# Optimization experiments

Measured on AMD Instinct MI355X. Metric: run time of the kernel, lower is better.

Reference implementation:

```python
import jax, jax.numpy as jnp
import numpy as np

B, N, K = 8192, 2048, 4  # batch, nodes, neighbors (original: 45, 168, 4)


def _collect_and_transfer(x, adj):
    # x: (B, N), adj: (N, K) int indices of neighbors.
    # Original builds, per node i, a (B, K) block of gathered neighbor values,
    # stacks to (N, B, K), then raw-reshapes (view) to (B, 1, K, N).
    g = jnp.transpose(x[:, adj], (1, 0, 2))   # (N, B, K)
    return g.reshape(x.shape[0], 1, K, adj.shape[0])  # memory reinterpretation, as in .view


def reference(x, label, adj, conv_w, conv_b, lin_w, lin_b):
    a = jnp.concatenate([_collect_and_transfer(x, adj),
                         _collect_and_transfer(label, adj)], axis=1)  # (B, 2, K, N)
    # Conv2d(2 -> 1, kernel=(1,4), stride=(1,4)): (B, 1, K, N//4)
    y = jax.lax.conv_general_dilated(
        a, conv_w, window_strides=(1, 4), padding='VALID',
        dimension_numbers=('NCHW', 'OIHW', 'NCHW'))
    y = jax.nn.relu(y + conv_b[None, :, None, None])
    y = y.reshape(B, N)              # K * (N//4) == N
    return y @ lin_w.T + lin_b       # Linear(N, N)


def setup_inputs() -> dict:
    key = jax.random.key(0)
    k1, k2, k3, k4, k5 = jax.random.split(key, 5)
    return {
        'x': jax.random.normal(k1, (B, N), dtype=jnp.float32),
        'label': jax.random.normal(k2, (B, N), dtype=jnp.float32),
        'adj': jax.random.randint(k3, (N, K), 0, N, dtype=jnp.int32),
        'conv_w': jax.random.normal(k4, (1, 2, 1, 4), dtype=jnp.float32) * 0.1,
        'conv_b': jnp.zeros((1,), dtype=jnp.float32),
        'lin_w': jax.random.normal(k5, (N, N), dtype=jnp.float32) * 0.02,
        'lin_b': jnp.zeros((N,), dtype=jnp.float32),
    }
```

## Files before the change

### kernel.cpp

```cpp
#include <hip/hip_runtime.h>

typedef __bf16 bf16;
typedef bf16 bf16x8 __attribute__((ext_vector_type(8)));
typedef float f32x4 __attribute__((ext_vector_type(4)));
typedef unsigned short ushort;
typedef ushort ushort4v __attribute__((ext_vector_type(4)));

#define BB 8192
#define NN 2048

__device__ __forceinline__ void async16(const void* g, void* l) {
    __builtin_amdgcn_global_load_lds(
        (__attribute__((address_space(1))) void*)(void*)g,
        (__attribute__((address_space(3))) void*)l,
        16, 0, 0);
}

__global__ __launch_bounds__(256) void conv_gather(
    const float* __restrict__ x, const float* __restrict__ label,
    const int* __restrict__ adj, const float* __restrict__ cw,
    const float* __restrict__ cb, bf16* __restrict__ V) {
    __shared__ float4 sxl[NN];
    const int bb0 = blockIdx.x * 2;
    const int t   = threadIdx.x;

    const float4* x0 = (const float4*)(x     + (size_t)bb0 * NN);
    const float4* x1 = (const float4*)(x     + (size_t)(bb0 + 1) * NN);
    const float4* l0 = (const float4*)(label + (size_t)bb0 * NN);
    const float4* l1 = (const float4*)(label + (size_t)(bb0 + 1) * NN);
#pragma unroll
    for (int q = 0; q < 2; ++q) {
        int i = q * 256 + t;
        float4 a = x0[i], b = l0[i], c = x1[i], d = l1[i];
        int n0i = i * 4;
        int sx  = (i >> 1) & 7;
        sxl[(n0i + 0) ^ sx] = make_float4(a.x, b.x, c.x, d.x);
        sxl[(n0i + 1) ^ sx] = make_float4(a.y, b.y, c.y, d.y);
        sxl[(n0i + 2) ^ sx] = make_float4(a.z, b.z, c.z, d.z);
        sxl[(n0i + 3) ^ sx] = make_float4(a.w, b.w, c.w, d.w);
    }
    const float w0 = cw[0], w1 = cw[1], w2 = cw[2], w3 = cw[3];
    const float w4 = cw[4], w5 = cw[5], w6 = cw[6], w7 = cw[7];
    const float bias = cb[0];

    const int4* adj4 = (const int4*)adj;
    int4 a[8];
#pragma unroll
    for (int j = 0; j < 8; ++j) a[j] = adj4[t * 8 + j];

    __syncthreads();

    bf16 o0[8], o1[8];
#pragma unroll
    for (int j = 0; j < 8; ++j) {
        int4 aa = a[j];
        float4 p0 = sxl[aa.x ^ ((aa.x >> 3) & 7)];
        float4 p1 = sxl[aa.y ^ ((aa.y >> 3) & 7)];
        float4 p2 = sxl[aa.z ^ ((aa.z >> 3) & 7)];
        float4 p3 = sxl[aa.w ^ ((aa.w >> 3) & 7)];
        float v0 = bias
                 + w0 * p0.x + w1 * p1.x + w2 * p2.x + w3 * p3.x
                 + w4 * p0.y + w5 * p1.y + w6 * p2.y + w7 * p3.y;
        float v1 = bias
                 + w0 * p0.z + w1 * p1.z + w2 * p2.z + w3 * p3.z
                 + w4 * p0.w + w5 * p1.w + w6 * p2.w + w7 * p3.w;
        o0[j] = (bf16)fmaxf(v0, 0.0f);
        o1[j] = (bf16)fmaxf(v1, 0.0f);
    }
    *(bf16x8*)(V + (size_t)bb0 * NN + t * 8)       = *(const bf16x8*)o0;
    *(bf16x8*)(V + (size_t)(bb0 + 1) * NN + t * 8) = *(const bf16x8*)o1;
}

__global__ __launch_bounds__(256) void transp_cvtw(
    const ushort* __restrict__ V, ushort* __restrict__ Y,
    const float* __restrict__ W, bf16* __restrict__ Wb) {
    const int b = blockIdx.x;
    if (b >= 4096) {
        size_t i = (size_t)(b - 4096) * 256 + threadIdx.x;
        float4 v0 = ((const float4*)W)[i * 2 + 0];
        float4 v1 = ((const float4*)W)[i * 2 + 1];
        bf16x8 o;
        o[0] = (bf16)v0.x; o[1] = (bf16)v0.y; o[2] = (bf16)v0.z; o[3] = (bf16)v0.w;
        o[4] = (bf16)v1.x; o[5] = (bf16)v1.y; o[6] = (bf16)v1.z; o[7] = (bf16)v1.w;
        ((bf16x8*)Wb)[i] = o;
        return;
    }
    __shared__ ushort tile[64][68];
    const int g0 = (b & 31) * 64;
    const int p0 = (b >> 5) * 64;
    const int c  = threadIdx.x & 15;
    const int r4 = threadIdx.x >> 4;

#pragma unroll
    for (int pass = 0; pass < 4; ++pass) {
        int r = pass * 16 + r4;
        ushort4v v = *(const ushort4v*)(V + (size_t)(p0 + r) * NN + g0 + c * 4);
        *(ushort4v*)&tile[r][c * 4] = v;
    }
    __syncthreads();
#pragma unroll
    for (int pass = 0; pass < 4; ++pass) {
        int r = pass * 16 + r4;
        ushort4v o;
        o.x = tile[c * 4 + 0][r];
        o.y = tile[c * 4 + 1][r];
        o.z = tile[c * 4 + 2][r];
        o.w = tile[c * 4 + 3][r];
        *(ushort4v*)(Y + (size_t)(g0 + r) * BB + p0 + c * 4) = o;
    }
}

__global__ __launch_bounds__(512, 2) void gemm_bt(
    const bf16* __restrict__ A, const bf16* __restrict__ W,
    const float* __restrict__ bias, float* __restrict__ out) {
    __shared__ __attribute__((aligned(16))) bf16 sA[2][16384];
    __shared__ __attribute__((aligned(16))) bf16 sB[2][16384];

    const int t    = threadIdx.x;
    const int lane = t & 63;
    const int wv   = t >> 6;
    const int wm   = wv & 1;
    const int wn   = wv >> 1;
    const int l16  = lane & 15;
    const int l4   = lane >> 4;

    const int bx = blockIdx.x >> 3;
    const int by = blockIdx.x & 7;
    const int m0 = bx * 256;
    const int n0 = by * 256;

    const int r8  = t >> 3;
    const int c8  = ((t & 7) ^ (r8 & 7)) * 8;
    const int dst = t * 8;

    const int sw    = l16 & 7;
    const int aOff0 = (wm * 128 + l16) * 64 + ((l4    ) ^ sw) * 8;
    const int aOff1 = (wm * 128 + l16) * 64 + ((l4 + 4) ^ sw) * 8;
    const int bOff0 = (wn * 64  + l16) * 64 + ((l4    ) ^ sw) * 8;
    const int bOff1 = (wn * 64  + l16) * 64 + ((l4 + 4) ^ sw) * 8;

    f32x4  acc[8][4] = {};
    bf16x8 aR[4][2], bR[4][2];

#define GBAR()  asm volatile("s_barrier" ::: "memory")
#define LGKM0() asm volatile("s_waitcnt lgkmcnt(0)" ::: "memory")
#define VMW4()  asm volatile("s_waitcnt vmcnt(4)" ::: "memory")
#define VMW0()  asm volatile("s_waitcnt vmcnt(0)" ::: "memory")

#define STG(G, rb, kt, lp) do {                                           \
        const bf16* _s = (G) + (size_t)((rb) + r8) * 2048 + (kt) + c8;    \
        async16(_s, (lp) + dst);                                          \
        async16(_s + (size_t)64 * 2048, (lp) + 4096 + dst);               \
    } while (0)

#define LDA(sp, mh) do {                                                  \
        const bf16* _p = (sp) + (mh) * 4096;                              \
        aR[0][0] = *(const bf16x8*)(_p + aOff0);                          \
        aR[0][1] = *(const bf16x8*)(_p + aOff1);                          \
        aR[1][0] = *(const bf16x8*)(_p + 1024 + aOff0);                   \
        aR[1][1] = *(const bf16x8*)(_p + 1024 + aOff1);                   \
        aR[2][0] = *(const bf16x8*)(_p + 2048 + aOff0);                   \
        aR[2][1] = *(const bf16x8*)(_p + 2048 + aOff1);                   \
        aR[3][0] = *(const bf16x8*)(_p + 3072 + aOff0);                   \
        aR[3][1] = *(const bf16x8*)(_p + 3072 + aOff1);                   \
    } while (0)

#define LDB(sp, nh) do {                                                  \
        const bf16* _p = (sp) + (nh) * 2048;                              \
        bR[(nh)*2+0][0] = *(const bf16x8*)(_p + bOff0);                   \
        bR[(nh)*2+0][1] = *(const bf16x8*)(_p + bOff1);                   \
        bR[(nh)*2+1][0] = *(const bf16x8*)(_p + 1024 + bOff0);            \
        bR[(nh)*2+1][1] = *(const bf16x8*)(_p + 1024 + bOff1);            \
    } while (0)

#define MM(mh, nh) do {                                                   \
        __builtin_amdgcn_s_setprio(1);                                    \
        _Pragma("unroll")                                                 \
        for (int _mf = 0; _mf < 4; ++_mf)                                 \
            _Pragma("unroll")                                             \
            for (int _nf = 0; _nf < 2; ++_nf) {                           \
                acc[(mh)*4+_mf][(nh)*2+_nf] =                             \
                    __builtin_amdgcn_mfma_f32_16x16x32_bf16(              \
                        aR[_mf][0], bR[(nh)*2+_nf][0],                    \
                        acc[(mh)*4+_mf][(nh)*2+_nf], 0, 0, 0);            \
                acc[(mh)*4+_mf][(nh)*2+_nf] =                             \
                    __builtin_amdgcn_mfma_f32_16x16x32_bf16(              \
                        aR[_mf][1], bR[(nh)*2+_nf][1],                    \
                        acc[(mh)*4+_mf][(nh)*2+_nf], 0, 0, 0);            \
            }                                                             \
        __builtin_amdgcn_s_setprio(0);                                    \
    } while (0)

    bf16* const sA0 = &sA[0][0]; bf16* const sA1 = &sA[1][0];
    bf16* const sB0 = &sB[0][0]; bf16* const sB1 = &sB[1][0];

    STG(A, m0,       0,  sA0);
    STG(A, m0 + 128, 0,  sA0 + 8192);
    STG(W, n0,       0,  sB0);
    STG(W, n0 + 128, 0,  sB0 + 8192);
    STG(W, n0,       64, sB1);
    STG(W, n0 + 128, 64, sB1 + 8192);
    VMW4();
    GBAR();

    for (int i = 0; i < 15; ++i) {
        const int kb = i * 128;
        LDA(sA0, 0); LDB(sB0, 0);
        STG(A, m0, kb + 64, sA1);
        GBAR(); LGKM0();
        MM(0, 0);
        GBAR();
        LDB(sB0, 1);
        STG(A, m0 + 128, kb + 64, sA1 + 8192);
        GBAR(); LGKM0();
        MM(0, 1);
        GBAR();
        LDA(sA0, 1);
        STG(W, n0, kb + 128, sB0);
        GBAR(); LGKM0();
        MM(1, 0);
        GBAR();
        STG(W, n0 + 128, kb + 128, sB0 + 8192);
        GBAR(); LGKM0();
        MM(1, 1);
        VMW4();
        GBAR();
        LDA(sA1, 0); LDB(sB1, 0);
        STG(A, m0, kb + 128, sA0);
        GBAR(); LGKM0();
        MM(0, 0);
        GBAR();
        LDB(sB1, 1);
        STG(A, m0 + 128, kb + 128, sA0 + 8192);
        GBAR(); LGKM0();
        MM(0, 1);
        GBAR();
        LDA(sA1, 1);
        STG(W, n0, kb + 192, sB1);
        GBAR(); LGKM0();
        MM(1, 0);
        GBAR();
        STG(W, n0 + 128, kb + 192, sB1 + 8192);
        GBAR(); LGKM0();
        MM(1, 1);
        VMW4();
        GBAR();
    }

    LDA(sA0, 0); LDB(sB0, 0);
    STG(A, m0, 1984, sA1);
    GBAR(); LGKM0(); MM(0, 0); GBAR();
    LDB(sB0, 1);
    STG(A, m0 + 128, 1984, sA1 + 8192);
    GBAR(); LGKM0(); MM(0, 1); GBAR();
    LDA(sA0, 1);
    GBAR(); LGKM0(); MM(1, 0); GBAR();
    GBAR(); LGKM0(); MM(1, 1);
    VMW0();
    GBAR();
    LDA(sA1, 0); LDB(sB1, 0);
    GBAR(); LGKM0(); MM(0, 0); GBAR();
    LDB(sB1, 1);
    GBAR(); LGKM0(); MM(0, 1); GBAR();
    LDA(sA1, 1);
    GBAR(); LGKM0(); MM(1, 0); GBAR();
    GBAR(); LGKM0(); MM(1, 1);

#pragma unroll
    for (int nf = 0; nf < 4; ++nf) {
        const int col = n0 + wn * 64 + nf * 16 + l16;
        const float bc = bias[col];
#pragma unroll
        for (int mf = 0; mf < 8; ++mf) {
            const size_t row = (size_t)(m0 + wm * 128 + mf * 16 + l4 * 4);
#pragma unroll
            for (int rr = 0; rr < 4; ++rr)
                out[(row + rr) * 2048 + col] = acc[mf][nf][rr] + bc;
        }
    }
#undef STG
#undef LDA
#undef LDB
#undef MM
#undef GBAR
#undef LGKM0
#undef VMW4
#undef VMW0
}

extern "C" void kernel_launch(void* const* d_in, const int* in_sizes, int n_in,
                              void* d_out, int out_size, void* d_ws, size_t ws_size,
                              hipStream_t stream) {
    (void)in_sizes; (void)n_in; (void)out_size; (void)ws_size;
    const float* x     = (const float*)d_in[0];
    const float* label = (const float*)d_in[1];
    const int*   adj   = (const int*)d_in[2];
    const float* cw    = (const float*)d_in[3];
    const float* cb    = (const float*)d_in[4];
    const float* lw    = (const float*)d_in[5];
    const float* lb    = (const float*)d_in[6];
    float* out = (float*)d_out;

    bf16* V  = (bf16*)d_out;
    bf16* Y2 = (bf16*)d_ws;
    bf16* Wb = (bf16*)((char*)d_ws + (size_t)2048 * 8192 * 2);

    conv_gather<<<BB / 2, 256, 0, stream>>>(x, label, adj, cw, cb, V);
    transp_cvtw<<<6144, 256, 0, stream>>>((const ushort*)V, (ushort*)Y2,
                                          lw, Wb);
    gemm_bt<<<dim3(256), 512, 0, stream>>>(Y2, Wb, lb, out);
}
```

Baseline: 278.7 us.

## Prefetch A tiles earlier, remap blocks per XCD, vectorize transpose LDS reads

The GEMM main loop now issues the next A-tile async loads one stage earlier, so the vmcnt wait threshold rises from 4 to 6 and more global loads stay in flight. Blocks are remapped so that each XCD processes a contiguous group of M rows, which aims for better L2 reuse of A. MFMA issue is reordered by k-slice, and a sched_barrier after each lgkmcnt wait pins the instruction schedule. The transpose kernel switches from scalar LDS reads to 4-wide vector reads and shuffles the values in registers. Together these aim to hide memory latency and cut LDS instruction count, at the cost of tighter ordering assumptions about outstanding loads.

```diff
diff --git a/kernel.cpp b/kernel.cpp
--- a/kernel.cpp
+++ b/kernel.cpp
@@ -85,7 +85,7 @@
         ((bf16x8*)Wb)[i] = o;
         return;
     }
-    __shared__ ushort tile[64][68];
+    __shared__ __attribute__((aligned(16))) ushort tile[64][68];
     const int g0 = (b & 31) * 64;
     const int p0 = (b >> 5) * 64;
     const int c  = threadIdx.x & 15;
@@ -98,15 +98,15 @@
         *(ushort4v*)&tile[r][c * 4] = v;
     }
     __syncthreads();
-#pragma unroll
-    for (int pass = 0; pass < 4; ++pass) {
-        int r = pass * 16 + r4;
+    ushort4v rv[4];
+#pragma unroll
+    for (int j = 0; j < 4; ++j)
+        rv[j] = *(const ushort4v*)&tile[c * 4 + j][r4 * 4];
+#pragma unroll
+    for (int q = 0; q < 4; ++q) {
         ushort4v o;
-        o.x = tile[c * 4 + 0][r];
-        o.y = tile[c * 4 + 1][r];
-        o.z = tile[c * 4 + 2][r];
-        o.w = tile[c * 4 + 3][r];
-        *(ushort4v*)(Y + (size_t)(g0 + r) * BB + p0 + c * 4) = o;
+        o.x = rv[0][q]; o.y = rv[1][q]; o.z = rv[2][q]; o.w = rv[3][q];
+        *(ushort4v*)(Y + (size_t)(g0 + r4 * 4 + q) * BB + p0 + c * 4) = o;
     }
 }
 
@@ -124,10 +124,12 @@
     const int l16  = lane & 15;
     const int l4   = lane >> 4;
 
-    const int bx = blockIdx.x >> 3;
-    const int by = blockIdx.x & 7;
-    const int m0 = bx * 256;
-    const int n0 = by * 256;
+    const int xcd = blockIdx.x & 7;
+    const int loc = blockIdx.x >> 3;
+    const int bx  = xcd * 4 + (loc >> 3);
+    const int by  = loc & 7;
+    const int m0  = bx * 256;
+    const int n0  = by * 256;
 
     const int r8  = t >> 3;
     const int c8  = ((t & 7) ^ (r8 & 7)) * 8;
@@ -143,8 +145,9 @@
     bf16x8 aR[4][2], bR[4][2];
 
 #define GBAR()  asm volatile("s_barrier" ::: "memory")
-#define LGKM0() asm volatile("s_waitcnt lgkmcnt(0)" ::: "memory")
-#define VMW4()  asm volatile("s_waitcnt vmcnt(4)" ::: "memory")
+#define LGKM0() do { asm volatile("s_waitcnt lgkmcnt(0)" ::: "memory"); \
+                     __builtin_amdgcn_sched_barrier(0); } while (0)
+#define VMW6()  asm volatile("s_waitcnt vmcnt(6)" ::: "memory")
 #define VMW0()  asm volatile("s_waitcnt vmcnt(0)" ::: "memory")
 
 #define STG(G, rb, kt, lp) do {                                           \
@@ -176,18 +179,15 @@
 #define MM(mh, nh) do {                                                   \
         __builtin_amdgcn_s_setprio(1);                                    \
         _Pragma("unroll")                                                 \
-        for (int _mf = 0; _mf < 4; ++_mf)                                 \
+        for (int _ks = 0; _ks < 2; ++_ks)                                 \
             _Pragma("unroll")                                             \
-            for (int _nf = 0; _nf < 2; ++_nf) {                           \
-                acc[(mh)*4+_mf][(nh)*2+_nf] =                             \
-                    __builtin_amdgcn_mfma_f32_16x16x32_bf16(              \
-                        aR[_mf][0], bR[(nh)*2+_nf][0],                    \
-                        acc[(mh)*4+_mf][(nh)*2+_nf], 0, 0, 0);            \
-                acc[(mh)*4+_mf][(nh)*2+_nf] =                             \
-                    __builtin_amdgcn_mfma_f32_16x16x32_bf16(              \
-                        aR[_mf][1], bR[(nh)*2+_nf][1],                    \
-                        acc[(mh)*4+_mf][(nh)*2+_nf], 0, 0, 0);            \
-            }                                                             \
+            for (int _mf = 0; _mf < 4; ++_mf)                             \
+                _Pragma("unroll")                                         \
+                for (int _nf = 0; _nf < 2; ++_nf)                         \
+                    acc[(mh)*4+_mf][(nh)*2+_nf] =                         \
+                        __builtin_amdgcn_mfma_f32_16x16x32_bf16(          \
+                            aR[_mf][_ks], bR[(nh)*2+_nf][_ks],            \
+                            acc[(mh)*4+_mf][(nh)*2+_nf], 0, 0, 0);        \
         __builtin_amdgcn_s_setprio(0);                                    \
     } while (0)
 
@@ -200,18 +200,18 @@
     STG(W, n0 + 128, 0,  sB0 + 8192);
     STG(W, n0,       64, sB1);
     STG(W, n0 + 128, 64, sB1 + 8192);
-    VMW4();
+    STG(A, m0,       64, sA1);
+    VMW6();
     GBAR();
 
     for (int i = 0; i < 15; ++i) {
         const int kb = i * 128;
         LDA(sA0, 0); LDB(sB0, 0);
-        STG(A, m0, kb + 64, sA1);
+        STG(A, m0 + 128, kb + 64, sA1 + 8192);
         GBAR(); LGKM0();
         MM(0, 0);
         GBAR();
         LDB(sB0, 1);
-        STG(A, m0 + 128, kb + 64, sA1 + 8192);
         GBAR(); LGKM0();
         MM(0, 1);
         GBAR();
@@ -221,17 +221,17 @@
         MM(1, 0);
         GBAR();
         STG(W, n0 + 128, kb + 128, sB0 + 8192);
+        STG(A, m0,       kb + 128, sA0);
         GBAR(); LGKM0();
         MM(1, 1);
-        VMW4();
+        VMW6();
         GBAR();
         LDA(sA1, 0); LDB(sB1, 0);
-        STG(A, m0, kb + 128, sA0);
+        STG(A, m0 + 128, kb + 128, sA0 + 8192);
         GBAR(); LGKM0();
         MM(0, 0);
         GBAR();
         LDB(sB1, 1);
-        STG(A, m0 + 128, kb + 128, sA0 + 8192);
         GBAR(); LGKM0();
         MM(0, 1);
         GBAR();
@@ -241,17 +241,17 @@
         MM(1, 0);
         GBAR();
         STG(W, n0 + 128, kb + 192, sB1 + 8192);
+        STG(A, m0,       kb + 192, sA1);
         GBAR(); LGKM0();
         MM(1, 1);
-        VMW4();
+        VMW6();
         GBAR();
     }
 
     LDA(sA0, 0); LDB(sB0, 0);
-    STG(A, m0, 1984, sA1);
+    STG(A, m0 + 128, 1984, sA1 + 8192);
     GBAR(); LGKM0(); MM(0, 0); GBAR();
     LDB(sB0, 1);
-    STG(A, m0 + 128, 1984, sA1 + 8192);
     GBAR(); LGKM0(); MM(0, 1); GBAR();
     LDA(sA0, 1);
     GBAR(); LGKM0(); MM(1, 0); GBAR();
@@ -284,7 +284,7 @@
 #undef MM
 #undef GBAR
 #undef LGKM0
-#undef VMW4
+#undef VMW6
 #undef VMW0
 }
 
```

Result: faster. 269.3 us (-3.4%).
